# Kernel tuning notes

Measured on AMD Instinct MI355X. Metric: run time of the kernel, lower is better.

## Reference

```python
import jax, jax.numpy as jnp
import numpy as np

STYLE_DIM = 512
NUM_DOMAINS = 8
BATCH = 16384
N_DEC_LAYERS = 4
N_EXP_LAYERS = 4   # each expert: Linear+ReLU x3, then Linear


def setup_inputs() -> dict:
    key = jax.random.key(0)
    ks = jax.random.split(key, 6)
    D, E, B = STYLE_DIM, NUM_DOMAINS, BATCH
    scale = 1.0 / np.sqrt(D)  # ~ torch Linear default init scale
    s = jax.random.normal(ks[0], (B, D), dtype=jnp.float32)
    y = jax.random.randint(ks[1], (B,), 0, E, dtype=jnp.int32)
    # decomposer params: stacked [L, out, in] / [L, out]
    dec_W = jax.random.uniform(ks[2], (N_DEC_LAYERS, D, D), jnp.float32, -scale, scale)
    dec_b = jax.random.uniform(ks[3], (N_DEC_LAYERS, D), jnp.float32, -scale, scale)
    # expert params: stacked [E, L, out, in] / [E, L, out]
    exp_W = jax.random.uniform(ks[4], (E, N_EXP_LAYERS, D, D), jnp.float32, -scale, scale)
    exp_b = jax.random.uniform(ks[5], (E, N_EXP_LAYERS, D), jnp.float32, -scale, scale)
    return {"s": s, "y": y, "dec_W": dec_W, "dec_b": dec_b, "exp_W": exp_W, "exp_b": exp_b}


def reference(s, y, dec_W, dec_b, exp_W, exp_b):
    h = s
    for l in range(N_DEC_LAYERS):
        h = jax.nn.relu(jnp.einsum('bi,oi->bo', h, dec_W[l]) + dec_b[l])
    s_unrelated = h                      # [B, D]
    s_related = s - s_unrelated          # [B, D]

    # run ALL experts on every sample (faithful to original dense compute)
    x = jnp.broadcast_to(s_related[:, None, :], (s.shape[0], NUM_DOMAINS, s.shape[1]))
    for l in range(N_EXP_LAYERS):
        x = jnp.einsum('bei,eoi->beo', x, exp_W[:, l]) + exp_b[:, l]
        if l < N_EXP_LAYERS - 1:
            x = jax.nn.relu(x)
    # gather the per-sample domain output: out[idx, y]
    s_related_tilde = jnp.take_along_axis(x, y[:, None, None].astype(jnp.int32), axis=1)[:, 0, :]
    s_tilde = s_related_tilde + s_unrelated
    return s_tilde
```

## Files before the change

### kernel.cpp

```cpp
#include <hip/hip_runtime.h>
#include <stdint.h>

#define BB 16384
#define PR2 16896
#define MAXT2 264

typedef short bf16x8 __attribute__((ext_vector_type(8)));
typedef float f32x4 __attribute__((ext_vector_type(4)));

typedef __attribute__((address_space(1))) unsigned short gus_t;
typedef __attribute__((address_space(3))) unsigned short lus_t;

__device__ __forceinline__ unsigned short f2bf(float f) {
    unsigned int u = __float_as_uint(f);
    u += 0x7fffu + ((u >> 16) & 1u);
    return (unsigned short)(u >> 16);
}
__device__ __forceinline__ float bf2f(unsigned short h) {
    return __uint_as_float(((unsigned int)h) << 16);
}

__device__ __forceinline__ void gld16(const unsigned short* g, unsigned short* l) {
    __builtin_amdgcn_global_load_lds(
        reinterpret_cast<const gus_t*>(reinterpret_cast<uintptr_t>(g)),
        reinterpret_cast<lus_t*>(reinterpret_cast<uintptr_t>(l)),
        16, 0, 0);
}

#define GLOAD(dst_, ptr_) \
    asm volatile("global_load_dwordx4 %0, %1, off" : "=v"(dst_) : "v"(ptr_) : "memory")

__global__ __launch_bounds__(256) void cvt_wt(const float* __restrict__ dec_W,
                                              const float* __restrict__ exp_W,
                                              unsigned short* __restrict__ dst) {
    const int g = blockIdx.x * 256 + threadIdx.x;
    const int li = g >> 15;
    const int r = g & 32767;
    const int col = r >> 6;
    const int ks = (r >> 2) & 15;
    const int kg = r & 3;
    const float* src = (li < 4 ? dec_W + ((size_t)li << 18)
                               : exp_W + ((size_t)(li - 4) << 18))
                     + (col << 9) + (ks << 5) + (kg << 3);
    f32x4 v0 = *reinterpret_cast<const f32x4*>(src);
    f32x4 v1 = *reinterpret_cast<const f32x4*>(src + 4);
    bf16x8 o;
#pragma unroll
    for (int q = 0; q < 4; ++q) { o[q] = (short)f2bf(v0[q]); o[q + 4] = (short)f2bf(v1[q]); }
    *reinterpret_cast<bf16x8*>(dst + ((size_t)li << 18) + (ks << 14) + (col << 5) + (kg << 3)) = o;
}

__global__ void bucket_init(int* perm, int* counts, int* cursors, int* tile_exp) {
    int i = blockIdx.x * blockDim.x + threadIdx.x;
    if (i < PR2) perm[i] = -1;
    if (i < 8) { counts[i] = 0; cursors[i] = 0; }
    if (i < MAXT2) tile_exp[i] = 0;
}

__global__ __launch_bounds__(1024) void bucket_count(const int* __restrict__ y, int* counts) {
    __shared__ int lc[8];
    const int t = threadIdx.x;
    if (t < 8) lc[t] = 0;
    __syncthreads();
    atomicAdd(&lc[y[blockIdx.x * 1024 + t]], 1);
    __syncthreads();
    if (t < 8) atomicAdd(&counts[t], lc[t]);
}

__global__ void bucket_scan(const int* __restrict__ counts, int* starts, int* tile_exp) {
    if (threadIdx.x == 0 && blockIdx.x == 0) {
        int s = 0;
        for (int e = 0; e < 8; ++e) {
            starts[e] = s;
            int nt = (counts[e] + 63) >> 6;
            for (int t = 0; t < nt; ++t) tile_exp[(s >> 6) + t] = e;
            s += nt << 6;
        }
        starts[8] = s;
    }
}

__global__ __launch_bounds__(1024) void bucket_scatter(const int* __restrict__ y,
                                                       const int* __restrict__ starts,
                                                       int* cursors, int* perm) {
    __shared__ int lc[8];
    __shared__ int lbase[8];
    const int t = threadIdx.x;
    if (t < 8) lc[t] = 0;
    __syncthreads();
    const int i = blockIdx.x * 1024 + t;
    const int e = y[i];
    const int r = atomicAdd(&lc[e], 1);
    __syncthreads();
    if (t < 8) lbase[t] = atomicAdd(&cursors[t], lc[t]);
    __syncthreads();
    perm[starts[e] + lbase[e] + r] = i;
}

#define MFMA8(afX, bvX)                                                              \
    acc[0][0] = __builtin_amdgcn_mfma_f32_16x16x32_bf16(afX##0, bvX[0], acc[0][0], 0, 0, 0); \
    acc[0][1] = __builtin_amdgcn_mfma_f32_16x16x32_bf16(afX##0, bvX[1], acc[0][1], 0, 0, 0); \
    acc[1][0] = __builtin_amdgcn_mfma_f32_16x16x32_bf16(afX##1, bvX[0], acc[1][0], 0, 0, 0); \
    acc[1][1] = __builtin_amdgcn_mfma_f32_16x16x32_bf16(afX##1, bvX[1], acc[1][1], 0, 0, 0); \
    acc[2][0] = __builtin_amdgcn_mfma_f32_16x16x32_bf16(afX##2, bvX[0], acc[2][0], 0, 0, 0); \
    acc[2][1] = __builtin_amdgcn_mfma_f32_16x16x32_bf16(afX##2, bvX[1], acc[2][1], 0, 0, 0); \
    acc[3][0] = __builtin_amdgcn_mfma_f32_16x16x32_bf16(afX##3, bvX[0], acc[3][0], 0, 0, 0); \
    acc[3][1] = __builtin_amdgcn_mfma_f32_16x16x32_bf16(afX##3, bvX[1], acc[3][1], 0, 0, 0);

template <int PHASE>
__global__ __launch_bounds__(1024) void fused4(
    const float* __restrict__ sf32,
    const unsigned short* __restrict__ srelg,
    const unsigned short* __restrict__ Wb,
    const float* __restrict__ biasb,
    unsigned short* __restrict__ srel_out,
    unsigned short* __restrict__ h_out,
    const unsigned short* __restrict__ h_in,
    float* __restrict__ outf,
    const int* __restrict__ perm,
    const int* __restrict__ tile_exp,
    const int* __restrict__ starts8)
{
    __shared__ __align__(16) unsigned short ls[32768];

    const int bid = blockIdx.x;
    int tile;
    if (PHASE == 0) {
        tile = ((bid & 7) << 5) + (bid >> 3);
    } else {
        tile = (bid & 7) * 33 + (bid >> 3);
        if ((tile << 6) >= starts8[0]) return;
    }

    const unsigned short* Wl;
    const float* bl;
    if (PHASE == 0) { Wl = Wb; bl = biasb; }
    else {
        const int e = tile_exp[tile];
        Wl = Wb + ((size_t)e << 20);
        bl = biasb + (e << 11);
    }

    const int t = threadIdx.x;
    const int w = t >> 6;
    const int lane = t & 63;
    const int lr = lane & 15;
    const int kg = lane >> 4;
    const int off = ((tile * 3) + w) & 15;

    const int ac = (t & 56) | ((t ^ w) & 7);
    const int axor = lr & 7;
    const int arow0 = ((0 << 4) + lr) << 9;
    const int arow1 = ((1 << 4) + lr) << 9;
    const int arow2 = ((2 << 4) + lr) << 9;
    const int arow3 = ((3 << 4) + lr) << 9;

    const unsigned short* wpt0 = Wl + ((((w << 5) + lr)) << 5) + (kg << 3);
    const unsigned short* wpt1 = wpt0 + 512;

    float bball[8];
#pragma unroll
    for (int l = 0; l < 4; ++l) {
        bball[(l << 1) + 0] = bl[(l << 9) + (w << 5) + lr];
        bball[(l << 1) + 1] = bl[(l << 9) + (w << 5) + 16 + lr];
    }

    if (PHASE == 0) {
#pragma unroll
        for (int c4 = 0; c4 < 4; ++c4) {
            const int grow = (tile << 6) + (c4 << 4) + w;
            const float* sp = sf32 + (((size_t)grow) << 9) + (ac << 3);
            f32x4 v0 = *reinterpret_cast<const f32x4*>(sp);
            f32x4 v1 = *reinterpret_cast<const f32x4*>(sp + 4);
            bf16x8 o;
#pragma unroll
            for (int q = 0; q < 4; ++q) { o[q] = (short)f2bf(v0[q]); o[q + 4] = (short)f2bf(v1[q]); }
            *reinterpret_cast<bf16x8*>(&ls[(c4 << 13) + (t << 3)]) = o;
        }
    } else {
#pragma unroll
        for (int c4 = 0; c4 < 4; ++c4) {
            int pr = perm[(tile << 6) + (c4 << 4) + w];
            if (pr < 0) pr = 0;
            gld16(srelg + (((size_t)pr) << 9) + (ac << 3), ls + (c4 << 13) + (t << 3));
        }
    }

    bf16x8 bv0[2], bv1[2];
    {
        const size_t l0 = ((size_t)(off & 15)) << 14;
        const size_t l1 = ((size_t)((1 + off) & 15)) << 14;
        GLOAD(bv0[0], wpt0 + l0); GLOAD(bv0[1], wpt1 + l0);
        GLOAD(bv1[0], wpt0 + l1); GLOAD(bv1[1], wpt1 + l1);
    }
    if (PHASE == 0) {
        asm volatile("s_waitcnt lgkmcnt(0)" ::: "memory");
    } else {
        asm volatile("s_waitcnt vmcnt(4)" ::: "memory");
    }
    __builtin_amdgcn_s_barrier();

    f32x4 acc[4][2];
#pragma unroll
    for (int m = 0; m < 4; ++m) { acc[m][0] = f32x4{0,0,0,0}; acc[m][1] = f32x4{0,0,0,0}; }

#define ITER(s_, bvS) do {                                                         \
    if ((s_) < 62) asm volatile("s_waitcnt vmcnt(2)" ::: "memory");                \
    else           asm volatile("s_waitcnt vmcnt(0)" ::: "memory");                \
    __builtin_amdgcn_sched_barrier(0);                                             \
    {                                                                              \
        const int st_ = (((s_) & 15) + off) & 15;                                  \
        const int sb_ = (st_ >> 1) << 6;                                           \
        const int klo_ = ((((st_ & 1) << 2) | kg) ^ axor) << 3;                    \
        bf16x8 af_0 = *reinterpret_cast<const bf16x8*>(&ls[arow0 + sb_ + klo_]);   \
        bf16x8 af_1 = *reinterpret_cast<const bf16x8*>(&ls[arow1 + sb_ + klo_]);   \
        bf16x8 af_2 = *reinterpret_cast<const bf16x8*>(&ls[arow2 + sb_ + klo_]);   \
        bf16x8 af_3 = *reinterpret_cast<const bf16x8*>(&ls[arow3 + sb_ + klo_]);   \
        MFMA8(af_, bvS)                                                            \
    }                                                                              \
    if ((s_) + 2 < 64) {                                                           \
        const size_t lofs_ = (((size_t)(((s_) + 2) >> 4)) << 18)                   \
                           + (((size_t)(((((s_) + 2) & 15) + off) & 15)) << 14);   \
        GLOAD(bvS[0], wpt0 + lofs_);                                               \
        GLOAD(bvS[1], wpt1 + lofs_);                                               \
    }                                                                              \
    if (((s_) & 15) == 15 && (s_) < 63) {                                          \
        __builtin_amdgcn_s_barrier();                \
        const int lb_ = ((s_) >> 4) << 1;                                          \
        _Pragma("unroll")                                                          \
        for (int m = 0; m < 4; ++m)                                                \
            _Pragma("unroll")                                                      \
            for (int j = 0; j < 2; ++j) {                                          \
                _Pragma("unroll")                                                  \
                for (int reg = 0; reg < 4; ++reg) {                                \
                    const int row_ = (m << 4) + (kg << 2) + reg;                   \
                    const float v_ = fmaxf(acc[m][j][reg] + bball[lb_ + j], 0.f);  \
                    const int c_ = (w << 2) + (j << 1) + (lr >> 3);                \
                    const int slot_ = (c_ & 56) | ((c_ ^ row_) & 7);               \
                    ls[(row_ << 9) + (slot_ << 3) + (lr & 7)] = f2bf(v_);          \
                }                                                                  \
                acc[m][j] = f32x4{0, 0, 0, 0};                                     \
            }                                                                      \
        asm volatile("s_waitcnt lgkmcnt(0)" ::: "memory");                         \
        __builtin_amdgcn_s_barrier();                                              \
    }                                                                              \
} while (0)

    for (int sp = 0; sp < 32; ++sp) {
        const int s0 = sp << 1;
        ITER(s0, bv0);
        ITER(s0 + 1, bv1);
    }
#undef ITER

    if (PHASE == 0) {
        __syncthreads();
#pragma unroll
        for (int m = 0; m < 4; ++m)
#pragma unroll
            for (int j = 0; j < 2; ++j)
#pragma unroll
                for (int reg = 0; reg < 4; ++reg) {
                    const int row = (m << 4) + (kg << 2) + reg;
                    const int col = (w << 5) + (j << 4) + lr;
                    const float h = fmaxf(acc[m][j][reg] + bball[6 + j], 0.f);
                    const float sv = sf32[(((size_t)((tile << 6) + row)) << 9) + col];
                    const int c = (w << 2) + (j << 1) + (lr >> 3);
                    const int slot = (c & 56) | ((c ^ row) & 7);
                    ls[(row << 9) + (slot << 3) + (lr & 7)] = f2bf(sv - h);
                }
        __syncthreads();
#pragma unroll
        for (int c4 = 0; c4 < 4; ++c4) {
            const int row = (c4 << 4) + w;
            const size_t go = (((size_t)((tile << 6) + row)) << 9) + (ac << 3);
            *reinterpret_cast<bf16x8*>(&srel_out[go]) =
                *reinterpret_cast<const bf16x8*>(&ls[(c4 << 13) + (t << 3)]);
        }
        __syncthreads();
#pragma unroll
        for (int m = 0; m < 4; ++m)
#pragma unroll
            for (int j = 0; j < 2; ++j)
#pragma unroll
                for (int reg = 0; reg < 4; ++reg) {
                    const int row = (m << 4) + (kg << 2) + reg;
                    const float h = fmaxf(acc[m][j][reg] + bball[6 + j], 0.f);
                    const int c = (w << 2) + (j << 1) + (lr >> 3);
                    const int slot = (c & 56) | ((c ^ row) & 7);
                    ls[(row << 9) + (slot << 3) + (lr & 7)] = f2bf(h);
                }
        __syncthreads();
#pragma unroll
        for (int c4 = 0; c4 < 4; ++c4) {
            const int row = (c4 << 4) + w;
            const size_t go = (((size_t)((tile << 6) + row)) << 9) + (ac << 3);
            *reinterpret_cast<bf16x8*>(&h_out[go]) =
                *reinterpret_cast<const bf16x8*>(&ls[(c4 << 13) + (t << 3)]);
        }
    } else {
#pragma unroll
        for (int m = 0; m < 4; ++m) {
#pragma unroll
            for (int reg = 0; reg < 4; ++reg) {
                const int row = (m << 4) + (kg << 2) + reg;
                const int pr = perm[(tile << 6) + row];
                if (pr >= 0) {
#pragma unroll
                    for (int j = 0; j < 2; ++j) {
                        const int col = (w << 5) + (j << 4) + lr;
                        const size_t gi = (((size_t)pr) << 9) + col;
                        outf[gi] = acc[m][j][reg] + bball[6 + j] + bf2f(h_in[gi]);
                    }
                }
            }
        }
    }
}

extern "C" void kernel_launch(void* const* d_in, const int* in_sizes, int n_in,
                              void* d_out, int out_size, void* d_ws, size_t ws_size,
                              hipStream_t stream)
{
    const float* s     = (const float*)d_in[0];
    const int*   y     = (const int*)d_in[1];
    const float* dec_W = (const float*)d_in[2];
    const float* dec_b = (const float*)d_in[3];
    const float* exp_W = (const float*)d_in[4];
    const float* exp_b = (const float*)d_in[5];
    float* out = (float*)d_out;

    unsigned short* Wt   = (unsigned short*)d_ws;
    unsigned short* srel = Wt + (size_t)36 * 262144;
    unsigned short* hbuf = srel + (size_t)BB * 512;
    int* perm     = (int*)(hbuf + (size_t)BB * 512);
    int* counts   = perm + PR2;
    int* cursors  = counts + 8;
    int* starts   = cursors + 8;
    int* tile_exp = starts + 9;

    cvt_wt<<<4608, 256, 0, stream>>>(dec_W, exp_W, Wt);

    bucket_init<<<(PR2 + 255) / 256, 256, 0, stream>>>(perm, counts, cursors, tile_exp);
    bucket_count<<<BB / 1024, 1024, 0, stream>>>(y, counts);
    bucket_scan<<<1, 64, 0, stream>>>(counts, starts, tile_exp);
    bucket_scatter<<<BB / 1024, 1024, 0, stream>>>(y, starts, cursors, perm);

    fused4<0><<<256, 1024, 0, stream>>>(s, nullptr, Wt, dec_b, srel, hbuf,
                                        nullptr, nullptr, nullptr, nullptr, nullptr);
    fused4<1><<<MAXT2, 1024, 0, stream>>>(nullptr, srel, Wt + ((size_t)4 << 18), exp_b,
                                          nullptr, nullptr, hbuf, out,
                                          perm, tile_exp, starts + 8);
}
```

Measured before the change: 164.7 us.

## Shrink row tile to 32 with 512-thread blocks and wider per-wave column tiles

The fused 4-layer MLP kernels now process 32-row tiles with 8 waves per block instead of 64-row tiles with 16 waves. Each wave covers 64 output columns (4 B fragments) across 2 M fragments, and bucket padding moves to 32-row granularity. Block count doubles and LDS per block halves, with launch bounds asking for 4 blocks per CU. This aims to cut padding waste in the expert phase and improve occupancy and load balance. The cost is that each weight fragment is reused across fewer rows, so weight traffic per output roughly doubles.

```diff
diff --git a/kernel.cpp b/kernel.cpp
--- a/kernel.cpp
+++ b/kernel.cpp
@@ -2,8 +2,8 @@
 #include <stdint.h>
 
 #define BB 16384
-#define PR2 16896
-#define MAXT2 264
+#define PR3 16640
+#define MAXT3 520
 
 typedef short bf16x8 __attribute__((ext_vector_type(8)));
 typedef float f32x4 __attribute__((ext_vector_type(4)));
@@ -52,9 +52,9 @@
 
 __global__ void bucket_init(int* perm, int* counts, int* cursors, int* tile_exp) {
     int i = blockIdx.x * blockDim.x + threadIdx.x;
-    if (i < PR2) perm[i] = -1;
+    if (i < PR3) perm[i] = -1;
     if (i < 8) { counts[i] = 0; cursors[i] = 0; }
-    if (i < MAXT2) tile_exp[i] = 0;
+    if (i < MAXT3) tile_exp[i] = 0;
 }
 
 __global__ __launch_bounds__(1024) void bucket_count(const int* __restrict__ y, int* counts) {
@@ -72,9 +72,9 @@
         int s = 0;
         for (int e = 0; e < 8; ++e) {
             starts[e] = s;
-            int nt = (counts[e] + 63) >> 6;
-            for (int t = 0; t < nt; ++t) tile_exp[(s >> 6) + t] = e;
-            s += nt << 6;
+            int nt = (counts[e] + 31) >> 5;
+            for (int t = 0; t < nt; ++t) tile_exp[(s >> 5) + t] = e;
+            s += nt << 5;
         }
         starts[8] = s;
     }
@@ -97,18 +97,18 @@
     perm[starts[e] + lbase[e] + r] = i;
 }
 
-#define MFMA8(afX, bvX)                                                              \
-    acc[0][0] = __builtin_amdgcn_mfma_f32_16x16x32_bf16(afX##0, bvX[0], acc[0][0], 0, 0, 0); \
-    acc[0][1] = __builtin_amdgcn_mfma_f32_16x16x32_bf16(afX##0, bvX[1], acc[0][1], 0, 0, 0); \
-    acc[1][0] = __builtin_amdgcn_mfma_f32_16x16x32_bf16(afX##1, bvX[0], acc[1][0], 0, 0, 0); \
-    acc[1][1] = __builtin_amdgcn_mfma_f32_16x16x32_bf16(afX##1, bvX[1], acc[1][1], 0, 0, 0); \
-    acc[2][0] = __builtin_amdgcn_mfma_f32_16x16x32_bf16(afX##2, bvX[0], acc[2][0], 0, 0, 0); \
-    acc[2][1] = __builtin_amdgcn_mfma_f32_16x16x32_bf16(afX##2, bvX[1], acc[2][1], 0, 0, 0); \
-    acc[3][0] = __builtin_amdgcn_mfma_f32_16x16x32_bf16(afX##3, bvX[0], acc[3][0], 0, 0, 0); \
-    acc[3][1] = __builtin_amdgcn_mfma_f32_16x16x32_bf16(afX##3, bvX[1], acc[3][1], 0, 0, 0);
+#define MFMA8(bvS)                                                                   \
+    acc[0][0] = __builtin_amdgcn_mfma_f32_16x16x32_bf16(af_0, bvS[0], acc[0][0], 0, 0, 0); \
+    acc[0][1] = __builtin_amdgcn_mfma_f32_16x16x32_bf16(af_0, bvS[1], acc[0][1], 0, 0, 0); \
+    acc[0][2] = __builtin_amdgcn_mfma_f32_16x16x32_bf16(af_0, bvS[2], acc[0][2], 0, 0, 0); \
+    acc[0][3] = __builtin_amdgcn_mfma_f32_16x16x32_bf16(af_0, bvS[3], acc[0][3], 0, 0, 0); \
+    acc[1][0] = __builtin_amdgcn_mfma_f32_16x16x32_bf16(af_1, bvS[0], acc[1][0], 0, 0, 0); \
+    acc[1][1] = __builtin_amdgcn_mfma_f32_16x16x32_bf16(af_1, bvS[1], acc[1][1], 0, 0, 0); \
+    acc[1][2] = __builtin_amdgcn_mfma_f32_16x16x32_bf16(af_1, bvS[2], acc[1][2], 0, 0, 0); \
+    acc[1][3] = __builtin_amdgcn_mfma_f32_16x16x32_bf16(af_1, bvS[3], acc[1][3], 0, 0, 0);
 
 template <int PHASE>
-__global__ __launch_bounds__(1024) void fused4(
+__global__ __launch_bounds__(512, 4) void fused4(
     const float* __restrict__ sf32,
     const unsigned short* __restrict__ srelg,
     const unsigned short* __restrict__ Wb,
@@ -121,15 +121,15 @@
     const int* __restrict__ tile_exp,
     const int* __restrict__ starts8)
 {
-    __shared__ __align__(16) unsigned short ls[32768];
+    __shared__ __align__(16) unsigned short ls[16384];
 
     const int bid = blockIdx.x;
     int tile;
     if (PHASE == 0) {
-        tile = ((bid & 7) << 5) + (bid >> 3);
+        tile = ((bid & 7) << 6) + (bid >> 3);
     } else {
-        tile = (bid & 7) * 33 + (bid >> 3);
-        if ((tile << 6) >= starts8[0]) return;
+        tile = (bid & 7) * 65 + (bid >> 3);
+        if ((tile << 5) >= starts8[0]) return;
     }
 
     const unsigned short* Wl;
@@ -148,64 +148,68 @@
     const int kg = lane >> 4;
     const int off = ((tile * 3) + w) & 15;
 
-    const int ac = (t & 56) | ((t ^ w) & 7);
+    const int ac = (lane & 56) | ((lane ^ w) & 7);
     const int axor = lr & 7;
-    const int arow0 = ((0 << 4) + lr) << 9;
-    const int arow1 = ((1 << 4) + lr) << 9;
-    const int arow2 = ((2 << 4) + lr) << 9;
-    const int arow3 = ((3 << 4) + lr) << 9;
-
-    const unsigned short* wpt0 = Wl + ((((w << 5) + lr)) << 5) + (kg << 3);
-    const unsigned short* wpt1 = wpt0 + 512;
-
-    float bball[8];
-#pragma unroll
-    for (int l = 0; l < 4; ++l) {
-        bball[(l << 1) + 0] = bl[(l << 9) + (w << 5) + lr];
-        bball[(l << 1) + 1] = bl[(l << 9) + (w << 5) + 16 + lr];
-    }
+    const int arow0 = (lr) << 9;
+    const int arow1 = ((16 + lr)) << 9;
+
+    const unsigned short* wpt[4];
+#pragma unroll
+    for (int j = 0; j < 4; ++j)
+        wpt[j] = Wl + (((w << 6) + (j << 4) + lr) << 5) + (kg << 3);
+
+    float bball[16];
+#pragma unroll
+    for (int l = 0; l < 4; ++l)
+#pragma unroll
+        for (int j = 0; j < 4; ++j)
+            bball[(l << 2) + j] = bl[(l << 9) + (w << 6) + (j << 4) + lr];
 
     if (PHASE == 0) {
 #pragma unroll
-        for (int c4 = 0; c4 < 4; ++c4) {
-            const int grow = (tile << 6) + (c4 << 4) + w;
+        for (int c2 = 0; c2 < 4; ++c2) {
+            const int grow = (tile << 5) + (c2 << 3) + w;
             const float* sp = sf32 + (((size_t)grow) << 9) + (ac << 3);
             f32x4 v0 = *reinterpret_cast<const f32x4*>(sp);
             f32x4 v1 = *reinterpret_cast<const f32x4*>(sp + 4);
             bf16x8 o;
 #pragma unroll
             for (int q = 0; q < 4; ++q) { o[q] = (short)f2bf(v0[q]); o[q + 4] = (short)f2bf(v1[q]); }
-            *reinterpret_cast<bf16x8*>(&ls[(c4 << 13) + (t << 3)]) = o;
+            *reinterpret_cast<bf16x8*>(&ls[(c2 << 12) + (t << 3)]) = o;
         }
     } else {
 #pragma unroll
-        for (int c4 = 0; c4 < 4; ++c4) {
-            int pr = perm[(tile << 6) + (c4 << 4) + w];
+        for (int c2 = 0; c2 < 4; ++c2) {
+            int pr = perm[(tile << 5) + (c2 << 3) + w];
             if (pr < 0) pr = 0;
-            gld16(srelg + (((size_t)pr) << 9) + (ac << 3), ls + (c4 << 13) + (t << 3));
-        }
-    }
-
-    bf16x8 bv0[2], bv1[2];
+            gld16(srelg + (((size_t)pr) << 9) + (ac << 3), ls + (c2 << 12) + (t << 3));
+        }
+    }
+
+    bf16x8 bv0[4], bv1[4];
     {
         const size_t l0 = ((size_t)(off & 15)) << 14;
         const size_t l1 = ((size_t)((1 + off) & 15)) << 14;
-        GLOAD(bv0[0], wpt0 + l0); GLOAD(bv0[1], wpt1 + l0);
-        GLOAD(bv1[0], wpt0 + l1); GLOAD(bv1[1], wpt1 + l1);
+        GLOAD(bv0[0], wpt[0] + l0); GLOAD(bv0[1], wpt[1] + l0);
+        GLOAD(bv0[2], wpt[2] + l0); GLOAD(bv0[3], wpt[3] + l0);
+        GLOAD(bv1[0], wpt[0] + l1); GLOAD(bv1[1], wpt[1] + l1);
+        GLOAD(bv1[2], wpt[2] + l1); GLOAD(bv1[3], wpt[3] + l1);
     }
     if (PHASE == 0) {
         asm volatile("s_waitcnt lgkmcnt(0)" ::: "memory");
     } else {
-        asm volatile("s_waitcnt vmcnt(4)" ::: "memory");
+        asm volatile("s_waitcnt vmcnt(8)" ::: "memory");
     }
     __builtin_amdgcn_s_barrier();
 
-    f32x4 acc[4][2];
-#pragma unroll
-    for (int m = 0; m < 4; ++m) { acc[m][0] = f32x4{0,0,0,0}; acc[m][1] = f32x4{0,0,0,0}; }
+    f32x4 acc[2][4];
+#pragma unroll
+    for (int m = 0; m < 2; ++m)
+#pragma unroll
+        for (int j = 0; j < 4; ++j) acc[m][j] = f32x4{0, 0, 0, 0};
 
 #define ITER(s_, bvS) do {                                                         \
-    if ((s_) < 62) asm volatile("s_waitcnt vmcnt(2)" ::: "memory");                \
+    if ((s_) < 62) asm volatile("s_waitcnt vmcnt(4)" ::: "memory");                \
     else           asm volatile("s_waitcnt vmcnt(0)" ::: "memory");                \
     __builtin_amdgcn_sched_barrier(0);                                             \
     {                                                                              \
@@ -214,28 +218,26 @@
         const int klo_ = ((((st_ & 1) << 2) | kg) ^ axor) << 3;                    \
         bf16x8 af_0 = *reinterpret_cast<const bf16x8*>(&ls[arow0 + sb_ + klo_]);   \
         bf16x8 af_1 = *reinterpret_cast<const bf16x8*>(&ls[arow1 + sb_ + klo_]);   \
-        bf16x8 af_2 = *reinterpret_cast<const bf16x8*>(&ls[arow2 + sb_ + klo_]);   \
-        bf16x8 af_3 = *reinterpret_cast<const bf16x8*>(&ls[arow3 + sb_ + klo_]);   \
-        MFMA8(af_, bvS)                                                            \
+        MFMA8(bvS)                                                                 \
     }                                                                              \
     if ((s_) + 2 < 64) {                                                           \
         const size_t lofs_ = (((size_t)(((s_) + 2) >> 4)) << 18)                   \
                            + (((size_t)(((((s_) + 2) & 15) + off) & 15)) << 14);   \
-        GLOAD(bvS[0], wpt0 + lofs_);                                               \
-        GLOAD(bvS[1], wpt1 + lofs_);                                               \
+        GLOAD(bvS[0], wpt[0] + lofs_); GLOAD(bvS[1], wpt[1] + lofs_);              \
+        GLOAD(bvS[2], wpt[2] + lofs_); GLOAD(bvS[3], wpt[3] + lofs_);              \
     }                                                                              \
     if (((s_) & 15) == 15 && (s_) < 63) {                                          \
         __builtin_amdgcn_s_barrier();                \
-        const int lb_ = ((s_) >> 4) << 1;                                          \
+        const int lb_ = ((s_) >> 4) << 2;                                          \
         _Pragma("unroll")                                                          \
-        for (int m = 0; m < 4; ++m)                                                \
+        for (int m = 0; m < 2; ++m)                                                \
             _Pragma("unroll")                                                      \
-            for (int j = 0; j < 2; ++j) {                                          \
+            for (int j = 0; j < 4; ++j) {                                          \
                 _Pragma("unroll")                                                  \
                 for (int reg = 0; reg < 4; ++reg) {                                \
                     const int row_ = (m << 4) + (kg << 2) + reg;                   \
                     const float v_ = fmaxf(acc[m][j][reg] + bball[lb_ + j], 0.f);  \
-                    const int c_ = (w << 2) + (j << 1) + (lr >> 3);                \
+                    const int c_ = (w << 3) + (j << 1) + (lr >> 3);                \
                     const int slot_ = (c_ & 56) | ((c_ ^ row_) & 7);               \
                     ls[(row_ << 9) + (slot_ << 3) + (lr & 7)] = f2bf(v_);          \
                 }                                                                  \
@@ -256,61 +258,61 @@
     if (PHASE == 0) {
         __syncthreads();
 #pragma unroll
-        for (int m = 0; m < 4; ++m)
-#pragma unroll
-            for (int j = 0; j < 2; ++j)
+        for (int m = 0; m < 2; ++m)
+#pragma unroll
+            for (int j = 0; j < 4; ++j)
 #pragma unroll
                 for (int reg = 0; reg < 4; ++reg) {
                     const int row = (m << 4) + (kg << 2) + reg;
-                    const int col = (w << 5) + (j << 4) + lr;
-                    const float h = fmaxf(acc[m][j][reg] + bball[6 + j], 0.f);
-                    const float sv = sf32[(((size_t)((tile << 6) + row)) << 9) + col];
-                    const int c = (w << 2) + (j << 1) + (lr >> 3);
+                    const int col = (w << 6) + (j << 4) + lr;
+                    const float h = fmaxf(acc[m][j][reg] + bball[12 + j], 0.f);
+                    const float sv = sf32[(((size_t)((tile << 5) + row)) << 9) + col];
+                    const int c = (w << 3) + (j << 1) + (lr >> 3);
                     const int slot = (c & 56) | ((c ^ row) & 7);
                     ls[(row << 9) + (slot << 3) + (lr & 7)] = f2bf(sv - h);
                 }
         __syncthreads();
 #pragma unroll
-        for (int c4 = 0; c4 < 4; ++c4) {
-            const int row = (c4 << 4) + w;
-            const size_t go = (((size_t)((tile << 6) + row)) << 9) + (ac << 3);
+        for (int c2 = 0; c2 < 4; ++c2) {
+            const int row = (c2 << 3) + w;
+            const size_t go = (((size_t)((tile << 5) + row)) << 9) + (ac << 3);
             *reinterpret_cast<bf16x8*>(&srel_out[go]) =
-                *reinterpret_cast<const bf16x8*>(&ls[(c4 << 13) + (t << 3)]);
+                *reinterpret_cast<const bf16x8*>(&ls[(c2 << 12) + (t << 3)]);
         }
         __syncthreads();
 #pragma unroll
-        for (int m = 0; m < 4; ++m)
-#pragma unroll
-            for (int j = 0; j < 2; ++j)
+        for (int m = 0; m < 2; ++m)
+#pragma unroll
+            for (int j = 0; j < 4; ++j)
 #pragma unroll
                 for (int reg = 0; reg < 4; ++reg) {
                     const int row = (m << 4) + (kg << 2) + reg;
-                    const float h = fmaxf(acc[m][j][reg] + bball[6 + j], 0.f);
-                    const int c = (w << 2) + (j << 1) + (lr >> 3);
+                    const float h = fmaxf(acc[m][j][reg] + bball[12 + j], 0.f);
+                    const int c = (w << 3) + (j << 1) + (lr >> 3);
                     const int slot = (c & 56) | ((c ^ row) & 7);
                     ls[(row << 9) + (slot << 3) + (lr & 7)] = f2bf(h);
                 }
         __syncthreads();
 #pragma unroll
-        for (int c4 = 0; c4 < 4; ++c4) {
-            const int row = (c4 << 4) + w;
-            const size_t go = (((size_t)((tile << 6) + row)) << 9) + (ac << 3);
+        for (int c2 = 0; c2 < 4; ++c2) {
+            const int row = (c2 << 3) + w;
+            const size_t go = (((size_t)((tile << 5) + row)) << 9) + (ac << 3);
             *reinterpret_cast<bf16x8*>(&h_out[go]) =
-                *reinterpret_cast<const bf16x8*>(&ls[(c4 << 13) + (t << 3)]);
+                *reinterpret_cast<const bf16x8*>(&ls[(c2 << 12) + (t << 3)]);
         }
     } else {
 #pragma unroll
-        for (int m = 0; m < 4; ++m) {
+        for (int m = 0; m < 2; ++m) {
 #pragma unroll
             for (int reg = 0; reg < 4; ++reg) {
                 const int row = (m << 4) + (kg << 2) + reg;
-                const int pr = perm[(tile << 6) + row];
+                const int pr = perm[(tile << 5) + row];
                 if (pr >= 0) {
 #pragma unroll
-                    for (int j = 0; j < 2; ++j) {
-                        const int col = (w << 5) + (j << 4) + lr;
+                    for (int j = 0; j < 4; ++j) {
+                        const int col = (w << 6) + (j << 4) + lr;
                         const size_t gi = (((size_t)pr) << 9) + col;
-                        outf[gi] = acc[m][j][reg] + bball[6 + j] + bf2f(h_in[gi]);
+                        outf[gi] = acc[m][j][reg] + bball[12 + j] + bf2f(h_in[gi]);
                     }
                 }
             }
@@ -334,21 +336,21 @@
     unsigned short* srel = Wt + (size_t)36 * 262144;
     unsigned short* hbuf = srel + (size_t)BB * 512;
     int* perm     = (int*)(hbuf + (size_t)BB * 512);
-    int* counts   = perm + PR2;
+    int* counts   = perm + PR3;
     int* cursors  = counts + 8;
     int* starts   = cursors + 8;
     int* tile_exp = starts + 9;
 
     cvt_wt<<<4608, 256, 0, stream>>>(dec_W, exp_W, Wt);
 
-    bucket_init<<<(PR2 + 255) / 256, 256, 0, stream>>>(perm, counts, cursors, tile_exp);
+    bucket_init<<<(PR3 + 255) / 256, 256, 0, stream>>>(perm, counts, cursors, tile_exp);
     bucket_count<<<BB / 1024, 1024, 0, stream>>>(y, counts);
     bucket_scan<<<1, 64, 0, stream>>>(counts, starts, tile_exp);
     bucket_scatter<<<BB / 1024, 1024, 0, stream>>>(y, starts, cursors, perm);
 
-    fused4<0><<<256, 1024, 0, stream>>>(s, nullptr, Wt, dec_b, srel, hbuf,
-                                        nullptr, nullptr, nullptr, nullptr, nullptr);
-    fused4<1><<<MAXT2, 1024, 0, stream>>>(nullptr, srel, Wt + ((size_t)4 << 18), exp_b,
-                                          nullptr, nullptr, hbuf, out,
-                                          perm, tile_exp, starts + 8);
-}
+    fused4<0><<<512, 512, 0, stream>>>(s, nullptr, Wt, dec_b, srel, hbuf,
+                                       nullptr, nullptr, nullptr, nullptr, nullptr);
+    fused4<1><<<MAXT3, 512, 0, stream>>>(nullptr, srel, Wt + ((size_t)4 << 18), exp_b,
+                                         nullptr, nullptr, hbuf, out,
+                                         perm, tile_exp, starts + 8);
+}
```

New measurement: 219.8 us. 1.33x slower.
